# Performance work log

Measured on AMD Instinct MI355X. Metric: run time of the kernel, lower is better.

Reference implementation:

```python
import jax, jax.numpy as jnp
import numpy as np

B, S, DIM = 2, 2048, 1024
H, DH = 16, 64
WIN = 512


def setup_inputs() -> dict:
    key = jax.random.key(0)
    k1, k2, k3 = jax.random.split(key, 3)
    x = jax.random.normal(k1, (B, S, DIM), dtype=jnp.float32)
    Wqkv = jax.random.normal(k2, (DIM, 3 * H * DH), dtype=jnp.float32) * (DIM ** -0.5)
    Wout = jax.random.normal(k3, (H * DH, DIM), dtype=jnp.float32) * ((H * DH) ** -0.5)
    return {"x": x, "Wqkv": Wqkv, "Wout": Wout}


def reference(x, Wqkv, Wout):
    b, s, _ = x.shape
    qkv = jnp.einsum('bsd,de->bse', x, Wqkv)  # (B,S,3*H*DH)
    q, k, v = jnp.split(qkv, 3, axis=-1)
    # -> (B,H,S,DH)
    q = q.reshape(b, s, H, DH).transpose(0, 2, 1, 3)
    k = k.reshape(b, s, H, DH).transpose(0, 2, 1, 3)
    v = v.reshape(b, s, H, DH).transpose(0, 2, 1, 3)
    scale = DH ** -0.5  # attention sees per-head dim
    scores = jnp.einsum('bhsd,bhtd->bhst', q, k) * scale  # dense (B,H,S,S)
    i = jnp.arange(s)[:, None]
    j = jnp.arange(s)[None, :]
    mask = (j >= i - WIN + 1) & (j <= i)  # causal sliding window
    mask_value = -jnp.finfo(scores.dtype).max
    scores = jnp.where(mask[None, None], scores, mask_value)
    attn = jax.nn.softmax(scores, axis=-1)
    out = jnp.einsum('bhst,bhtd->bhsd', attn, v)
    out = out.transpose(0, 2, 1, 3).reshape(b, s, H * DH)
    return jnp.einsum('bse,ed->bsd', out, Wout)
```

## Files before the change

### kernel.cpp

```cpp
#include <hip/hip_runtime.h>

#define S_LEN 2048
#define BATCH 2
#define HDIM 1024
#define NH 16
#define DH 64
#define WINSZ 512
#define MROWS (BATCH * S_LEN)

typedef __attribute__((ext_vector_type(8))) short bfrag;
typedef __attribute__((ext_vector_type(4))) float f32x4;
typedef __attribute__((ext_vector_type(4))) int i128;

__device__ __forceinline__ short f2bf(float f) {
    union { float f; unsigned u; } v;
    v.f = f;
    unsigned r = v.u + 0x7fffu + ((v.u >> 16) & 1u);
    return (short)(r >> 16);
}

__device__ __forceinline__ void gload_lds16(const short* g, short* l) {
    __builtin_amdgcn_global_load_lds(
        (const __attribute__((address_space(1))) unsigned int*)g,
        (__attribute__((address_space(3))) unsigned int*)l, 16, 0, 0);
}

__global__ void cast_bf_kernel(const float* __restrict__ in, short* __restrict__ out, int n4) {
    int i = blockIdx.x * blockDim.x + threadIdx.x;
    if (i < n4) {
        float4 v = ((const float4*)in)[i];
        union { short s[4]; int2 p; } u;
        u.s[0] = f2bf(v.x); u.s[1] = f2bf(v.y); u.s[2] = f2bf(v.z); u.s[3] = f2bf(v.w);
        ((int2*)out)[i] = u.p;
    }
}

__global__ void transpose_cast_kernel(const float* __restrict__ in, short* __restrict__ out,
                                      int R, int C) {
    __shared__ float tile[32][33];
    int tc0 = blockIdx.x * 32;
    int tr0 = blockIdx.y * 32;
    int t = threadIdx.x;
    int c = t & 31, r0 = t >> 5;
    #pragma unroll
    for (int k = 0; k < 4; ++k) {
        int r = r0 + k * 8;
        tile[r][c] = in[(size_t)(tr0 + r) * C + tc0 + c];
    }
    __syncthreads();
    int r2 = t & 31, c0 = t >> 5;
    #pragma unroll
    for (int k = 0; k < 4; ++k) {
        int c2 = c0 + k * 8;
        out[(size_t)(tc0 + c2) * R + tr0 + r2] = f2bf(tile[r2][c2]);
    }
}

__global__ __launch_bounds__(256, 2)
void gemm_bt(const short* __restrict__ A, const short* __restrict__ Bt,
             int M, int N, int K, int mode,
             short* __restrict__ cbf, float* __restrict__ co)
{
    __shared__ __align__(16) short Al[2][128 * 32];
    __shared__ __align__(16) short Bl[2][128 * 32];
    const int t = threadIdx.x;
    const int lane = t & 63;
    const int wave = t >> 6;
    const int wr = wave >> 1, wc = wave & 1;
    const int m0 = blockIdx.y * 128, n0 = blockIdx.x * 128;
    const int lrow = lane & 15;
    const int lk8 = (lane >> 4) << 3;

    f32x4 acc[4][4];
    #pragma unroll
    for (int m = 0; m < 4; ++m)
        #pragma unroll
        for (int n = 0; n < 4; ++n)
            acc[m][n] = (f32x4){0.f, 0.f, 0.f, 0.f};

    const int row0s = t >> 2, col0s = (t & 3) << 3;
    const int row1s = (256 + t) >> 2, col1s = (t & 3) << 3;
    const size_t dst0 = (size_t)(wave * 64) * 8;
    const size_t dst1 = (size_t)(256 + wave * 64) * 8;

    auto stage = [&](int k0, int sb) {
        gload_lds16(&A[(size_t)(m0 + row0s) * K + k0 + col0s], &Al[sb][0] + dst0);
        gload_lds16(&Bt[(size_t)(n0 + row0s) * K + k0 + col0s], &Bl[sb][0] + dst0);
        gload_lds16(&A[(size_t)(m0 + row1s) * K + k0 + col1s], &Al[sb][0] + dst1);
        gload_lds16(&Bt[(size_t)(n0 + row1s) * K + k0 + col1s], &Bl[sb][0] + dst1);
    };

    const int nk = K >> 5;
    stage(0, 0);
    __syncthreads();
    for (int ki = 0; ki < nk; ++ki) {
        const int cur = ki & 1;
        if (ki + 1 < nk) stage((ki + 1) << 5, cur ^ 1);
        bfrag af[4], bfr[4];
        #pragma unroll
        for (int m = 0; m < 4; ++m)
            af[m] = *(const bfrag*)(&Al[cur][(wr * 64 + m * 16 + lrow) * 32 + lk8]);
        #pragma unroll
        for (int n = 0; n < 4; ++n)
            bfr[n] = *(const bfrag*)(&Bl[cur][(wc * 64 + n * 16 + lrow) * 32 + lk8]);
        #pragma unroll
        for (int m = 0; m < 4; ++m)
            #pragma unroll
            for (int n = 0; n < 4; ++n)
                acc[m][n] = __builtin_amdgcn_mfma_f32_16x16x32_bf16(af[m], bfr[n], acc[m][n], 0, 0, 0);
        __syncthreads();
    }

    if (mode == 1) {
        #pragma unroll
        for (int m = 0; m < 4; ++m)
            #pragma unroll
            for (int n = 0; n < 4; ++n) {
                int col = n0 + wc * 64 + n * 16 + lrow;
                int row0 = m0 + wr * 64 + m * 16 + ((lane >> 4) << 2);
                #pragma unroll
                for (int r = 0; r < 4; ++r)
                    co[(size_t)(row0 + r) * N + col] = acc[m][n][r];
            }
    } else {
        #pragma unroll
        for (int m = 0; m < 4; ++m)
            #pragma unroll
            for (int n = 0; n < 4; ++n) {
                int col = n0 + wc * 64 + n * 16 + lrow;
                int row0 = m0 + wr * 64 + m * 16 + ((lane >> 4) << 2);
                #pragma unroll
                for (int r = 0; r < 4; ++r)
                    cbf[(size_t)(row0 + r) * N + col] = f2bf(acc[m][n][r]);
            }
    }
}

__global__ __launch_bounds__(256)
void vtr_kernel(const short* __restrict__ qkv, short* __restrict__ vt) {
    __shared__ __align__(16) short tile[64][72];
    const int bh = blockIdx.x >> 5;
    const int s0 = (blockIdx.x & 31) << 6;
    const int b = bh >> 4, h = bh & 15;
    const short* src = qkv + (size_t)b * S_LEN * 3072 + 2048 + h * 64;
    const int t = threadIdx.x;
    const int sl = t >> 2, dh0 = (t & 3) << 4;
    *(i128*)&tile[sl][dh0]     = *(const i128*)&src[(size_t)(s0 + sl) * 3072 + dh0];
    *(i128*)&tile[sl][dh0 + 8] = *(const i128*)&src[(size_t)(s0 + sl) * 3072 + dh0 + 8];
    __syncthreads();
    const int dhl = t >> 2, sc = (t & 3) << 4;
    union { short sh[8]; i128 v; } u0, u1;
    #pragma unroll
    for (int i = 0; i < 8; ++i) { u0.sh[i] = tile[sc + i][dhl]; u1.sh[i] = tile[sc + 8 + i][dhl]; }
    short* dst = vt + ((size_t)bh * DH + dhl) * S_LEN + s0 + sc;
    *(i128*)&dst[0] = u0.v;
    *(i128*)&dst[8] = u1.v;
}

__global__ __launch_bounds__(256, 4)
void attn_kernel(const short* __restrict__ qkv, const short* __restrict__ vt,
                 short* __restrict__ attno)
{
    __shared__ __align__(16) short Kl[2][64 * 64];
    __shared__ __align__(16) short Vl[2][64 * 64];
    __shared__ __align__(16) short Pl[4][16 * 64];

    const int bid = blockIdx.x;
    const int logical = (bid & 7) * 128 + (bid >> 3);
    const int qblk = logical & 31;
    const int bh = logical >> 5;
    const int b = bh >> 4, h = bh & 15;

    const int t = threadIdx.x;
    const int wave = t >> 6, lane = t & 63;
    const int qb0 = qblk * 64;
    const int i0 = qb0 + wave * 16;
    const short* qbase = qkv + (size_t)b * S_LEN * 3072 + h * 64;
    const short* kbase = qkv + (size_t)b * S_LEN * 3072 + 1024 + h * 64;
    const short* vp = vt + (size_t)bh * DH * S_LEN;
    char* myP = (char*)&Pl[wave][0];

    const int lq = lane & 15;
    const int g = lane >> 4;
    const int swz = (lq & 7) << 4;
    const int l7 = lq & 7;

    bfrag qf[2];
    qf[0] = *(const bfrag*)(&qbase[(size_t)(i0 + lq) * 3072 + (g << 3)]);
    qf[1] = *(const bfrag*)(&qbase[(size_t)(i0 + lq) * 3072 + 32 + (g << 3)]);

    f32x4 oacc[4];
    #pragma unroll
    for (int d = 0; d < 4; ++d) oacc[d] = (f32x4){0.f, 0.f, 0.f, 0.f};
    float m2 = -1e30f, lrun = 0.f;
    const float QSCALE = 0.125f * 1.44269504f;
    const int qi = i0 + lq;

    int j_lo = qb0 - (WINSZ - 1);
    if (j_lo < 0) j_lo = 0;
    j_lo &= ~63;
    const int nT = ((qb0 + 64) - j_lo) >> 6;

    auto stage = [&](int j0, short* kbuf, short* vbuf) {
        #pragma unroll
        for (int qq = 0; qq < 2; ++qq) {
            int chunk = qq * 256 + wave * 64 + lane;
            int row = chunk >> 3;
            int cc = (chunk & 7) ^ (row & 7);
            short* kdst = kbuf + (size_t)(qq * 256 + wave * 64) * 8;
            short* vdst = vbuf + (size_t)(qq * 256 + wave * 64) * 8;
            gload_lds16(kbase + (size_t)(j_lo + j0 + row) * 3072 + cc * 8, kdst);
            gload_lds16(vp + (size_t)row * S_LEN + j_lo + j0 + cc * 8, vdst);
        }
    };

    stage(0, Kl[0], Vl[0]);
    __syncthreads();

    for (int ti = 0; ti < nT; ++ti) {
        const int cur = ti & 1;
        const int j0 = j_lo + ti * 64;
        if (ti + 1 < nT) stage((ti + 1) * 64, Kl[cur ^ 1], Vl[cur ^ 1]);

        const short* Kc = Kl[cur];
        const short* Vc = Vl[cur];

        f32x4 sc[4];
        #pragma unroll
        for (int tc = 0; tc < 4; ++tc) {
            bfrag a0 = *(const bfrag*)(&Kc[(tc * 16 + lq) * 64 + ((g ^ l7) << 3)]);
            bfrag a1 = *(const bfrag*)(&Kc[(tc * 16 + lq) * 64 + (((4 | g) ^ l7) << 3)]);
            f32x4 z = (f32x4){0.f, 0.f, 0.f, 0.f};
            z = __builtin_amdgcn_mfma_f32_16x16x32_bf16(a0, qf[0], z, 0, 0, 0);
            z = __builtin_amdgcn_mfma_f32_16x16x32_bf16(a1, qf[1], z, 0, 0, 0);
            sc[tc] = z;
        }

        const bool nomask = (j0 >= i0 - (WINSZ - 16)) && (j0 + 63 <= i0);
        float s[4][4];
        float pm = -1e30f;
        #pragma unroll
        for (int tc = 0; tc < 4; ++tc)
            #pragma unroll
            for (int r = 0; r < 4; ++r) {
                float sv = sc[tc][r] * QSCALE;
                if (!nomask) {
                    int kj = j0 + tc * 16 + 4 * g + r;
                    sv = ((kj <= qi) && (kj > qi - WINSZ)) ? sv : -1e30f;
                }
                s[tc][r] = sv;
                pm = fmaxf(pm, sv);
            }
        pm = fmaxf(pm, __shfl_xor(pm, 16));
        pm = fmaxf(pm, __shfl_xor(pm, 32));
        float mnew = fmaxf(m2, pm);
        float scale_old = exp2f(m2 - mnew);
        m2 = mnew;
        float p[4][4];
        float rs = 0.f;
        #pragma unroll
        for (int tc = 0; tc < 4; ++tc)
            #pragma unroll
            for (int r = 0; r < 4; ++r) {
                p[tc][r] = exp2f(s[tc][r] - mnew);
                rs += p[tc][r];
            }
        rs += __shfl_xor(rs, 16);
        rs += __shfl_xor(rs, 32);
        lrun = lrun * scale_old + rs;
        #pragma unroll
        for (int d = 0; d < 4; ++d) {
            f32x4 o = oacc[d];
            o[0] *= scale_old; o[1] *= scale_old; o[2] *= scale_old; o[3] *= scale_old;
            oacc[d] = o;
        }

        #pragma unroll
        for (int tc = 0; tc < 4; ++tc) {
            union { short sh[4]; int2 w; } u;
            u.sh[0] = f2bf(p[tc][0]); u.sh[1] = f2bf(p[tc][1]);
            u.sh[2] = f2bf(p[tc][2]); u.sh[3] = f2bf(p[tc][3]);
            int wb = (lq * 128 + tc * 32 + g * 8) ^ swz;
            *(int2*)(myP + wb) = u.w;
        }
        asm volatile("s_waitcnt lgkmcnt(0)" ::: "memory");

        #pragma unroll
        for (int kt = 0; kt < 2; ++kt) {
            int rb = (lq * 128 + kt * 64 + g * 16) ^ swz;
            bfrag pf = *(const bfrag*)(myP + rb);
            #pragma unroll
            for (int d = 0; d < 4; ++d) {
                bfrag vfr = *(const bfrag*)(&Vc[(d * 16 + lq) * 64 + (((kt * 4 + g) ^ l7) << 3)]);
                oacc[d] = __builtin_amdgcn_mfma_f32_16x16x32_bf16(vfr, pf, oacc[d], 0, 0, 0);
            }
        }
        __syncthreads();
    }

    const float inv_l = 1.f / lrun;
    size_t rowbase = ((size_t)(b * S_LEN + qi)) * HDIM + h * DH;
    #pragma unroll
    for (int d = 0; d < 4; ++d) {
        union { short sh[4]; int2 w; } u;
        #pragma unroll
        for (int r = 0; r < 4; ++r)
            u.sh[r] = f2bf(oacc[d][r] * inv_l);
        *(int2*)(&attno[rowbase + d * 16 + 4 * g]) = u.w;
    }
}

extern "C" void kernel_launch(void* const* d_in, const int* in_sizes, int n_in,
                              void* d_out, int out_size, void* d_ws, size_t ws_size,
                              hipStream_t stream) {
    const float* x = (const float*)d_in[0];
    const float* Wqkv = (const float*)d_in[1];
    const float* Wout = (const float*)d_in[2];
    float* out = (float*)d_out;
    char* ws = (char*)d_ws;

    short* x_bf   = (short*)(ws);
    short* wqkv_t = (short*)(ws + 8388608);
    short* wout_t = (short*)(ws + 14680064);
    short* qkv_rm = (short*)(ws + 16777216);
    short* v_t    = (short*)(ws + 41943040);
    short* attno  = x_bf;

    cast_bf_kernel<<<4096, 256, 0, stream>>>(x, x_bf, MROWS * HDIM / 4);
    transpose_cast_kernel<<<dim3(96, 32), 256, 0, stream>>>(Wqkv, wqkv_t, 1024, 3072);
    transpose_cast_kernel<<<dim3(32, 32), 256, 0, stream>>>(Wout, wout_t, 1024, 1024);

    gemm_bt<<<dim3(24, 32), 256, 0, stream>>>(x_bf, wqkv_t, MROWS, 3 * HDIM, HDIM, 0,
                                              qkv_rm, nullptr);
    vtr_kernel<<<1024, 256, 0, stream>>>(qkv_rm, v_t);
    attn_kernel<<<dim3(BATCH * NH * (S_LEN / 64)), 256, 0, stream>>>(qkv_rm, v_t, attno);
    gemm_bt<<<dim3(8, 32), 256, 0, stream>>>(attno, wout_t, MROWS, HDIM, HDIM, 1,
                                             nullptr, out);
}
```

Before: 175.0 us.

## Fuse V transpose into QKV GEMM epilogue, merge prep kernels, add MFMA priority

After: 166.6 us. -4.8%, faster.

```diff
diff --git a/kernel.cpp b/kernel.cpp
--- a/kernel.cpp
+++ b/kernel.cpp
@@ -25,22 +25,37 @@
         (__attribute__((address_space(3))) unsigned int*)l, 16, 0, 0);
 }
 
-__global__ void cast_bf_kernel(const float* __restrict__ in, short* __restrict__ out, int n4) {
-    int i = blockIdx.x * blockDim.x + threadIdx.x;
-    if (i < n4) {
-        float4 v = ((const float4*)in)[i];
+__global__ __launch_bounds__(256)
+void prep_kernel(const float* __restrict__ x, const float* __restrict__ Wqkv,
+                 const float* __restrict__ Wout,
+                 short* __restrict__ x_bf, short* __restrict__ wqkv_t, short* __restrict__ wout_t)
+{
+    __shared__ float tile[32][33];
+    const int bid = blockIdx.x;
+    const int t = threadIdx.x;
+
+    if (bid < 4096) {
+        int i = bid * 256 + t;
+        float4 v = ((const float4*)x)[i];
         union { short s[4]; int2 p; } u;
         u.s[0] = f2bf(v.x); u.s[1] = f2bf(v.y); u.s[2] = f2bf(v.z); u.s[3] = f2bf(v.w);
-        ((int2*)out)[i] = u.p;
-    }
-}
-
-__global__ void transpose_cast_kernel(const float* __restrict__ in, short* __restrict__ out,
-                                      int R, int C) {
-    __shared__ float tile[32][33];
-    int tc0 = blockIdx.x * 32;
-    int tr0 = blockIdx.y * 32;
-    int t = threadIdx.x;
+        ((int2*)x_bf)[i] = u.p;
+        return;
+    }
+
+    const float* in;
+    short* out;
+    int R, C, bx, by;
+    if (bid < 7168) {
+        int lb = bid - 4096;
+        in = Wqkv; out = wqkv_t; R = 1024; C = 3072;
+        bx = lb % 96; by = lb / 96;
+    } else {
+        int lb = bid - 7168;
+        in = Wout; out = wout_t; R = 1024; C = 1024;
+        bx = lb & 31; by = lb >> 5;
+    }
+    int tc0 = bx * 32, tr0 = by * 32;
     int c = t & 31, r0 = t >> 5;
     #pragma unroll
     for (int k = 0; k < 4; ++k) {
@@ -57,19 +72,21 @@
 }
 
 __global__ __launch_bounds__(256, 2)
-void gemm_bt(const short* __restrict__ A, const short* __restrict__ Bt,
-             int M, int N, int K, int mode,
-             short* __restrict__ cbf, float* __restrict__ co)
+void gemm_qkv(const short* __restrict__ A, const short* __restrict__ Bt,
+              short* __restrict__ qk_rm, short* __restrict__ vto)
 {
-    __shared__ __align__(16) short Al[2][128 * 32];
-    __shared__ __align__(16) short Bl[2][128 * 32];
+    __shared__ __align__(16) short smraw[17408];
+    short (*Al)[4096] = (short(*)[4096])smraw;
+    short (*Bl)[4096] = (short(*)[4096])(smraw + 8192);
+    const int K = HDIM;
     const int t = threadIdx.x;
     const int lane = t & 63;
     const int wave = t >> 6;
     const int wr = wave >> 1, wc = wave & 1;
     const int m0 = blockIdx.y * 128, n0 = blockIdx.x * 128;
-    const int lrow = lane & 15;
-    const int lk8 = (lane >> 4) << 3;
+    const int lq = lane & 15;
+    const int g = lane >> 4;
+    const int lk8 = g << 3;
 
     f32x4 acc[4][4];
     #pragma unroll
@@ -79,15 +96,15 @@
             acc[m][n] = (f32x4){0.f, 0.f, 0.f, 0.f};
 
     const int row0s = t >> 2, col0s = (t & 3) << 3;
-    const int row1s = (256 + t) >> 2, col1s = (t & 3) << 3;
+    const int row1s = (256 + t) >> 2;
     const size_t dst0 = (size_t)(wave * 64) * 8;
     const size_t dst1 = (size_t)(256 + wave * 64) * 8;
 
     auto stage = [&](int k0, int sb) {
         gload_lds16(&A[(size_t)(m0 + row0s) * K + k0 + col0s], &Al[sb][0] + dst0);
         gload_lds16(&Bt[(size_t)(n0 + row0s) * K + k0 + col0s], &Bl[sb][0] + dst0);
-        gload_lds16(&A[(size_t)(m0 + row1s) * K + k0 + col1s], &Al[sb][0] + dst1);
-        gload_lds16(&Bt[(size_t)(n0 + row1s) * K + k0 + col1s], &Bl[sb][0] + dst1);
+        gload_lds16(&A[(size_t)(m0 + row1s) * K + k0 + col0s], &Al[sb][0] + dst1);
+        gload_lds16(&Bt[(size_t)(n0 + row1s) * K + k0 + col0s], &Bl[sb][0] + dst1);
     };
 
     const int nk = K >> 5;
@@ -99,10 +116,10 @@
         bfrag af[4], bfr[4];
         #pragma unroll
         for (int m = 0; m < 4; ++m)
-            af[m] = *(const bfrag*)(&Al[cur][(wr * 64 + m * 16 + lrow) * 32 + lk8]);
+            af[m] = *(const bfrag*)(&Al[cur][(wr * 64 + m * 16 + lq) * 32 + lk8]);
         #pragma unroll
         for (int n = 0; n < 4; ++n)
-            bfr[n] = *(const bfrag*)(&Bl[cur][(wc * 64 + n * 16 + lrow) * 32 + lk8]);
+            bfr[n] = *(const bfrag*)(&Bl[cur][(wc * 64 + n * 16 + lq) * 32 + lk8]);
         #pragma unroll
         for (int m = 0; m < 4; ++m)
             #pragma unroll
@@ -111,54 +128,115 @@
         __syncthreads();
     }
 
-    if (mode == 1) {
+    if (n0 < 2048) {
         #pragma unroll
         for (int m = 0; m < 4; ++m)
             #pragma unroll
             for (int n = 0; n < 4; ++n) {
-                int col = n0 + wc * 64 + n * 16 + lrow;
-                int row0 = m0 + wr * 64 + m * 16 + ((lane >> 4) << 2);
+                int col = n0 + wc * 64 + n * 16 + lq;
+                int row0 = m0 + wr * 64 + m * 16 + g * 4;
                 #pragma unroll
                 for (int r = 0; r < 4; ++r)
-                    co[(size_t)(row0 + r) * N + col] = acc[m][n][r];
+                    qk_rm[(size_t)(row0 + r) * 2048 + col] = f2bf(acc[m][n][r]);
             }
     } else {
+        short* T = smraw;
         #pragma unroll
         for (int m = 0; m < 4; ++m)
             #pragma unroll
             for (int n = 0; n < 4; ++n) {
-                int col = n0 + wc * 64 + n * 16 + lrow;
-                int row0 = m0 + wr * 64 + m * 16 + ((lane >> 4) << 2);
+                int cl = wc * 64 + n * 16 + lq;
+                int rl0 = wr * 64 + m * 16 + g * 4;
+                union { short sh[4]; int2 w; } u;
                 #pragma unroll
-                for (int r = 0; r < 4; ++r)
-                    cbf[(size_t)(row0 + r) * N + col] = f2bf(acc[m][n][r]);
+                for (int r = 0; r < 4; ++r) u.sh[r] = f2bf(acc[m][n][r]);
+                *(int2*)(&T[cl * 136 + rl0]) = u.w;
             }
-    }
-}
-
-__global__ __launch_bounds__(256)
-void vtr_kernel(const short* __restrict__ qkv, short* __restrict__ vt) {
-    __shared__ __align__(16) short tile[64][72];
-    const int bh = blockIdx.x >> 5;
-    const int s0 = (blockIdx.x & 31) << 6;
-    const int b = bh >> 4, h = bh & 15;
-    const short* src = qkv + (size_t)b * S_LEN * 3072 + 2048 + h * 64;
+        __syncthreads();
+        const int b = m0 >> 11, sbase = m0 & 2047;
+        const int h0 = (n0 - 2048) >> 6;
+        #pragma unroll
+        for (int i = 0; i < 8; ++i) {
+            int c2 = i * 256 + t;
+            int rv = c2 >> 4;
+            int sc = (c2 & 15) << 3;
+            int h = h0 + (rv >> 6), dh = rv & 63;
+            i128 v = *(const i128*)(&T[rv * 136 + sc]);
+            *(i128*)(&vto[((size_t)((b * NH + h) * DH + dh)) * S_LEN + sbase + sc]) = v;
+        }
+    }
+}
+
+__global__ __launch_bounds__(256, 2)
+void gemm_out(const short* __restrict__ A, const short* __restrict__ Bt,
+              float* __restrict__ co)
+{
+    __shared__ __align__(16) short Al[2][128 * 32];
+    __shared__ __align__(16) short Bl[2][128 * 32];
+    const int K = HDIM, N = HDIM;
     const int t = threadIdx.x;
-    const int sl = t >> 2, dh0 = (t & 3) << 4;
-    *(i128*)&tile[sl][dh0]     = *(const i128*)&src[(size_t)(s0 + sl) * 3072 + dh0];
-    *(i128*)&tile[sl][dh0 + 8] = *(const i128*)&src[(size_t)(s0 + sl) * 3072 + dh0 + 8];
+    const int lane = t & 63;
+    const int wave = t >> 6;
+    const int wr = wave >> 1, wc = wave & 1;
+    const int m0 = blockIdx.y * 128, n0 = blockIdx.x * 128;
+    const int lq = lane & 15;
+    const int g = lane >> 4;
+    const int lk8 = g << 3;
+
+    f32x4 acc[4][4];
+    #pragma unroll
+    for (int m = 0; m < 4; ++m)
+        #pragma unroll
+        for (int n = 0; n < 4; ++n)
+            acc[m][n] = (f32x4){0.f, 0.f, 0.f, 0.f};
+
+    const int row0s = t >> 2, col0s = (t & 3) << 3;
+    const int row1s = (256 + t) >> 2;
+    const size_t dst0 = (size_t)(wave * 64) * 8;
+    const size_t dst1 = (size_t)(256 + wave * 64) * 8;
+
+    auto stage = [&](int k0, int sb) {
+        gload_lds16(&A[(size_t)(m0 + row0s) * K + k0 + col0s], &Al[sb][0] + dst0);
+        gload_lds16(&Bt[(size_t)(n0 + row0s) * K + k0 + col0s], &Bl[sb][0] + dst0);
+        gload_lds16(&A[(size_t)(m0 + row1s) * K + k0 + col0s], &Al[sb][0] + dst1);
+        gload_lds16(&Bt[(size_t)(n0 + row1s) * K + k0 + col0s], &Bl[sb][0] + dst1);
+    };
+
+    const int nk = K >> 5;
+    stage(0, 0);
     __syncthreads();
-    const int dhl = t >> 2, sc = (t & 3) << 4;
-    union { short sh[8]; i128 v; } u0, u1;
-    #pragma unroll
-    for (int i = 0; i < 8; ++i) { u0.sh[i] = tile[sc + i][dhl]; u1.sh[i] = tile[sc + 8 + i][dhl]; }
-    short* dst = vt + ((size_t)bh * DH + dhl) * S_LEN + s0 + sc;
-    *(i128*)&dst[0] = u0.v;
-    *(i128*)&dst[8] = u1.v;
+    for (int ki = 0; ki < nk; ++ki) {
+        const int cur = ki & 1;
+        if (ki + 1 < nk) stage((ki + 1) << 5, cur ^ 1);
+        bfrag af[4], bfr[4];
+        #pragma unroll
+        for (int m = 0; m < 4; ++m)
+            af[m] = *(const bfrag*)(&Al[cur][(wr * 64 + m * 16 + lq) * 32 + lk8]);
+        #pragma unroll
+        for (int n = 0; n < 4; ++n)
+            bfr[n] = *(const bfrag*)(&Bl[cur][(wc * 64 + n * 16 + lq) * 32 + lk8]);
+        #pragma unroll
+        for (int m = 0; m < 4; ++m)
+            #pragma unroll
+            for (int n = 0; n < 4; ++n)
+                acc[m][n] = __builtin_amdgcn_mfma_f32_16x16x32_bf16(af[m], bfr[n], acc[m][n], 0, 0, 0);
+        __syncthreads();
+    }
+
+    #pragma unroll
+    for (int m = 0; m < 4; ++m)
+        #pragma unroll
+        for (int n = 0; n < 4; ++n) {
+            int col = n0 + wc * 64 + n * 16 + lq;
+            int row0 = m0 + wr * 64 + m * 16 + g * 4;
+            #pragma unroll
+            for (int r = 0; r < 4; ++r)
+                co[(size_t)(row0 + r) * N + col] = acc[m][n][r];
+        }
 }
 
 __global__ __launch_bounds__(256, 4)
-void attn_kernel(const short* __restrict__ qkv, const short* __restrict__ vt,
+void attn_kernel(const short* __restrict__ qk, const short* __restrict__ vt,
                  short* __restrict__ attno)
 {
     __shared__ __align__(16) short Kl[2][64 * 64];
@@ -175,8 +253,8 @@
     const int wave = t >> 6, lane = t & 63;
     const int qb0 = qblk * 64;
     const int i0 = qb0 + wave * 16;
-    const short* qbase = qkv + (size_t)b * S_LEN * 3072 + h * 64;
-    const short* kbase = qkv + (size_t)b * S_LEN * 3072 + 1024 + h * 64;
+    const short* qbase = qk + (size_t)b * S_LEN * 2048 + h * 64;
+    const short* kbase = qk + (size_t)b * S_LEN * 2048 + 1024 + h * 64;
     const short* vp = vt + (size_t)bh * DH * S_LEN;
     char* myP = (char*)&Pl[wave][0];
 
@@ -186,8 +264,8 @@
     const int l7 = lq & 7;
 
     bfrag qf[2];
-    qf[0] = *(const bfrag*)(&qbase[(size_t)(i0 + lq) * 3072 + (g << 3)]);
-    qf[1] = *(const bfrag*)(&qbase[(size_t)(i0 + lq) * 3072 + 32 + (g << 3)]);
+    qf[0] = *(const bfrag*)(&qbase[(size_t)(i0 + lq) * 2048 + (g << 3)]);
+    qf[1] = *(const bfrag*)(&qbase[(size_t)(i0 + lq) * 2048 + 32 + (g << 3)]);
 
     f32x4 oacc[4];
     #pragma unroll
@@ -209,7 +287,7 @@
             int cc = (chunk & 7) ^ (row & 7);
             short* kdst = kbuf + (size_t)(qq * 256 + wave * 64) * 8;
             short* vdst = vbuf + (size_t)(qq * 256 + wave * 64) * 8;
-            gload_lds16(kbase + (size_t)(j_lo + j0 + row) * 3072 + cc * 8, kdst);
+            gload_lds16(kbase + (size_t)(j_lo + j0 + row) * 2048 + cc * 8, kdst);
             gload_lds16(vp + (size_t)row * S_LEN + j_lo + j0 + cc * 8, vdst);
         }
     };
@@ -226,6 +304,7 @@
         const short* Vc = Vl[cur];
 
         f32x4 sc[4];
+        __builtin_amdgcn_s_setprio(1);
         #pragma unroll
         for (int tc = 0; tc < 4; ++tc) {
             bfrag a0 = *(const bfrag*)(&Kc[(tc * 16 + lq) * 64 + ((g ^ l7) << 3)]);
@@ -235,6 +314,7 @@
             z = __builtin_amdgcn_mfma_f32_16x16x32_bf16(a1, qf[1], z, 0, 0, 0);
             sc[tc] = z;
         }
+        __builtin_amdgcn_s_setprio(0);
 
         const bool nomask = (j0 >= i0 - (WINSZ - 16)) && (j0 + 63 <= i0);
         float s[4][4];
@@ -285,6 +365,7 @@
         }
         asm volatile("s_waitcnt lgkmcnt(0)" ::: "memory");
 
+        __builtin_amdgcn_s_setprio(1);
         #pragma unroll
         for (int kt = 0; kt < 2; ++kt) {
             int rb = (lq * 128 + kt * 64 + g * 16) ^ swz;
@@ -295,6 +376,7 @@
                 oacc[d] = __builtin_amdgcn_mfma_f32_16x16x32_bf16(vfr, pf, oacc[d], 0, 0, 0);
             }
         }
+        __builtin_amdgcn_s_setprio(0);
         __syncthreads();
     }
 
@@ -322,18 +404,12 @@
     short* x_bf   = (short*)(ws);
     short* wqkv_t = (short*)(ws + 8388608);
     short* wout_t = (short*)(ws + 14680064);
-    short* qkv_rm = (short*)(ws + 16777216);
-    short* v_t    = (short*)(ws + 41943040);
+    short* qk_rm  = (short*)(ws + 16777216);
+    short* v_t    = (short*)(ws + 33554432);
     short* attno  = x_bf;
 
-    cast_bf_kernel<<<4096, 256, 0, stream>>>(x, x_bf, MROWS * HDIM / 4);
-    transpose_cast_kernel<<<dim3(96, 32), 256, 0, stream>>>(Wqkv, wqkv_t, 1024, 3072);
-    transpose_cast_kernel<<<dim3(32, 32), 256, 0, stream>>>(Wout, wout_t, 1024, 1024);
-
-    gemm_bt<<<dim3(24, 32), 256, 0, stream>>>(x_bf, wqkv_t, MROWS, 3 * HDIM, HDIM, 0,
-                                              qkv_rm, nullptr);
-    vtr_kernel<<<1024, 256, 0, stream>>>(qkv_rm, v_t);
-    attn_kernel<<<dim3(BATCH * NH * (S_LEN / 64)), 256, 0, stream>>>(qkv_rm, v_t, attno);
-    gemm_bt<<<dim3(8, 32), 256, 0, stream>>>(attno, wout_t, MROWS, HDIM, HDIM, 1,
-                                             nullptr, out);
-}
+    prep_kernel<<<8192, 256, 0, stream>>>(x, Wqkv, Wout, x_bf, wqkv_t, wout_t);
+    gemm_qkv<<<dim3(24, 32), 256, 0, stream>>>(x_bf, wqkv_t, qk_rm, v_t);
+    attn_kernel<<<dim3(BATCH * NH * (S_LEN / 64)), 256, 0, stream>>>(qk_rm, v_t, attno);
+    gemm_out<<<dim3(8, 32), 256, 0, stream>>>(attno, wout_t, out);
+}
```
